# Performance work log

Measured on AMD Instinct MI355X. Metric: run time of the kernel, lower is better.

Reference implementation:

```python
import jax, jax.numpy as jnp
import numpy as np

N_DEPTH = 4
N_STACKS = 2
INPUT_SIZE = 1024
HIDDEN_SIZE = 4096
HU = HIDDEN_SIZE // (N_DEPTH * N_STACKS)  # unit_hidden_size = 512
BATCH = 4096


def setup_inputs() -> dict:
    key = jax.random.key(0)
    ks = jax.random.split(key, 8)
    inp = {
        "input": jax.random.normal(ks[0], (BATCH, INPUT_SIZE), dtype=jnp.float32),
        "state": jax.random.normal(ks[1], (2, N_STACKS, BATCH, HIDDEN_SIZE), dtype=jnp.float32),
        # LSTMCell params; residualStack=True -> every cell input dim = INPUT_SIZE
        "W_ih": jax.random.normal(ks[2], (N_DEPTH, N_STACKS, 4 * HU, INPUT_SIZE), dtype=jnp.float32) * 0.05,
        "W_hh": jax.random.normal(ks[3], (N_DEPTH, N_STACKS, 4 * HU, HU), dtype=jnp.float32) * 0.05,
        "b_ih": jax.random.normal(ks[4], (N_DEPTH, N_STACKS, 4 * HU), dtype=jnp.float32) * 0.05,
        "b_hh": jax.random.normal(ks[5], (N_DEPTH, N_STACKS, 4 * HU), dtype=jnp.float32) * 0.05,
        # stacks_proj: Linear(HU, INPUT_SIZE)
        "proj_W": jax.random.normal(ks[6], (INPUT_SIZE, HU), dtype=jnp.float32) * 0.05,
        "proj_b": jax.random.normal(ks[7], (INPUT_SIZE,), dtype=jnp.float32) * 0.05,
    }
    return inp


def _lstm_cell(x, hx, cx, w_ih, w_hh, b_ih, b_hh):
    # gates: [B, 4*HU], PyTorch LSTMCell gate order: i, f, g, o
    gates = x @ w_ih.T + b_ih + hx @ w_hh.T + b_hh
    i_g, f_g, g_g, o_g = jnp.split(gates, 4, axis=-1)
    i_g = jax.nn.sigmoid(i_g)
    f_g = jax.nn.sigmoid(f_g)
    g_g = jnp.tanh(g_g)
    o_g = jax.nn.sigmoid(o_g)
    c_out = f_g * cx + i_g * g_g
    h_out = o_g * jnp.tanh(c_out)
    return h_out, c_out


def reference(input, state, W_ih, W_hh, b_ih, b_hh, proj_W, proj_b):
    # residual=True, residualStack=True
    h_depth, c_depth = [], []
    for i in range(N_DEPTH):
        s, e = i * HU, (i + 1) * HU
        hs, cs = [], []
        dec_input = input
        h_out = None
        for j in range(N_STACKS):
            if j > 0:
                # residualStack: dec_input = dec_input + stacks_proj(h_out)
                dec_input = dec_input + h_out @ proj_W.T + proj_b
            hx = state[0, j, :, s:e]
            cx = state[1, j, :, s:e]
            h_out, c_out = _lstm_cell(dec_input, hx, cx,
                                      W_ih[i, j], W_hh[i, j], b_ih[i, j], b_hh[i, j])
            hs.append(h_out + hx)  # residual=True
            cs.append(c_out)
        h_depth.append(jnp.stack(hs, 0))  # [nStacks, B, HU]
        c_depth.append(jnp.stack(cs, 0))
    # hidden dim is laid out by depth slice: newState[..., i*HU:(i+1)*HU]
    newH = jnp.concatenate(h_depth, axis=-1)  # [nStacks, B, hidden_size]
    newC = jnp.concatenate(c_depth, axis=-1)
    newState = jnp.stack([newH, newC], axis=0)  # [2, nStacks, B, hidden_size]
    ho = newState[0, -1]  # [B, hidden_size]
    return ho, newState
```

## Files before the change

kernel.cpp:

```cpp
#include <hip/hip_runtime.h>
#include <cstdint>
#include <cstddef>

#define B_   4096
#define ISZ  1024
#define SW   4096
#define OHW  2048
#define HU_  512
#define NG   2048

typedef float f32x4 __attribute__((ext_vector_type(4)));
typedef short bf16x8 __attribute__((ext_vector_type(8)));

__device__ __forceinline__ short f2bf(float x) {
    union { float f; unsigned u; } v; v.f = x;
    unsigned r = v.u + 0x7fffu + ((v.u >> 16) & 1u);
    return (short)(r >> 16);
}
__device__ __forceinline__ float sigm(float x)   { return 1.f / (1.f + __expf(-x)); }
__device__ __forceinline__ float tanh_f(float x) { return 2.f / (1.f + __expf(-2.f * x)) - 1.f; }

__device__ __forceinline__ void async16(const void* g, void* l) {
    __builtin_amdgcn_global_load_lds((__attribute__((address_space(1))) void*)g,
                                     (__attribute__((address_space(3))) void*)l,
                                     16, 0, 0);
}

#define VM_BAR(N) asm volatile("s_waitcnt vmcnt(" #N ")\n\ts_barrier" ::: "memory")
#define BAR()     __builtin_amdgcn_s_barrier()

__global__ __launch_bounds__(256) void cvt_kernel(const float* __restrict__ src,
                                                  short* __restrict__ dst, long n) {
    long i = ((long)blockIdx.x * 256 + threadIdx.x) * 8;
    if (i >= n) return;
    float4 a = *(const float4*)(src + i);
    float4 b = *(const float4*)(src + i + 4);
    bf16x8 o;
    o[0] = f2bf(a.x); o[1] = f2bf(a.y); o[2] = f2bf(a.z); o[3] = f2bf(a.w);
    o[4] = f2bf(b.x); o[5] = f2bf(b.y); o[6] = f2bf(b.z); o[7] = f2bf(b.w);
    *(bf16x8*)(dst + i) = o;
}

__global__ __launch_bounds__(256) void cvt_h_kernel(const float* __restrict__ src,
                                                    short* __restrict__ dst) {
    long i = ((long)blockIdx.x * 256 + threadIdx.x) * 8;
    long row = i >> 11;
    long c   = i & 2047;
    const float* s = src + row * SW + c;
    float4 a = *(const float4*)(s);
    float4 b = *(const float4*)(s + 4);
    bf16x8 o;
    o[0] = f2bf(a.x); o[1] = f2bf(a.y); o[2] = f2bf(a.z); o[3] = f2bf(a.w);
    o[4] = f2bf(b.x); o[5] = f2bf(b.y); o[6] = f2bf(b.z); o[7] = f2bf(b.w);
    *(bf16x8*)(dst + i) = o;
}

#define MMA_BLK(BB, AR0, N0)                                                      \
  do {                                                                            \
    __builtin_amdgcn_s_setprio(1);                                                \
    _Pragma("unroll")                                                             \
    for (int mtl = 0; mtl < 4; ++mtl) {                                           \
      _Pragma("unroll")                                                           \
      for (int nn = 0; nn < 2; ++nn) {                                            \
        _Pragma("unroll")                                                         \
        for (int ks = 0; ks < 2; ++ks) {                                          \
          acc[(AR0) + mtl][(N0) + nn] = __builtin_amdgcn_mfma_f32_16x16x32_bf16(  \
              aR[mtl][ks], BB[nn][ks], acc[(AR0) + mtl][(N0) + nn], 0, 0, 0);     \
        }                                                                         \
      }                                                                           \
    }                                                                             \
    __builtin_amdgcn_s_setprio(0);                                                \
  } while (0)

#define GROW(rb) (((((rb) >> 4) & 3) << 9) + h0 + ((((rb) >> 6)) << 4) + ((rb) & 15))

__global__ __launch_bounds__(512, 2) void gates2_kernel(
    const short* __restrict__ A1, long a1_dstride,
    const short* __restrict__ Hb,
    const short* __restrict__ Wihb, const short* __restrict__ Whhb,
    const float* __restrict__ b_ih, const float* __restrict__ b_hh,
    const float* __restrict__ state,
    float* __restrict__ out_ho, float* __restrict__ out_state,
    short* __restrict__ h0b,
    int j)
{
    extern __shared__ short lds[];

    const int tid  = threadIdx.x;
    const int wave = tid >> 6;
    const int lane = tid & 63;
    const int wm   = wave >> 2;
    const int wn   = wave & 3;
    const int ln16 = lane & 15;
    const int q    = (lane >> 4) & 3;

    const int id  = blockIdx.x;
    const int swz = (id & 7) * 64 + (id >> 3);
    const int M0  = (swz & 15) * 256;
    const int h0  = ((swz >> 4) & 7) * 64;
    const int d   = swz >> 7;
    const int s   = d * HU_;

    const short* A1d = A1 + (size_t)d * a1_dstride;
    const short* A2  = Hb + (size_t)j * B_ * OHW + s;
    const short* W1  = Wihb + (size_t)(d * 2 + j) * NG * ISZ;
    const short* W2  = Whhb + (size_t)(d * 2 + j) * NG * HU_;
    const float* bi_ = b_ih + (size_t)(d * 2 + j) * NG;
    const float* bh_ = b_hh + (size_t)(d * 2 + j) * NG;

    const int srow = tid >> 3;
    const int scol = (((tid & 7) ^ ((tid >> 3) & 7)) << 3);

    const short* As = A1d;
    const short* Bs = W1;
    unsigned aoff0 = (unsigned)((M0 +   0 + srow) * ISZ + scol);
    unsigned aoff1 = (unsigned)((M0 +  64 + srow) * ISZ + scol);
    unsigned aoff2 = (unsigned)((M0 + 128 + srow) * ISZ + scol);
    unsigned aoff3 = (unsigned)((M0 + 192 + srow) * ISZ + scol);
    unsigned boff0 = (unsigned)(GROW(      srow) * ISZ + scol);
    unsigned boff1 = (unsigned)(GROW( 64 + srow) * ISZ + scol);
    unsigned boff2 = (unsigned)(GROW(128 + srow) * ISZ + scol);
    unsigned boff3 = (unsigned)(GROW(192 + srow) * ISZ + scol);

    const int swz0 = ((q    ) ^ (ln16 & 7)) << 4;
    const int swz1 = ((q + 4) ^ (ln16 & 7)) << 4;
    const char* ldsb = (const char*)lds;

    f32x4 acc[8][4];
#pragma unroll
    for (int i = 0; i < 8; ++i)
#pragma unroll
        for (int n = 0; n < 4; ++n) acc[i][n] = (f32x4){0.f, 0.f, 0.f, 0.f};

    bf16x8 aR[4][2];
    bf16x8 b01[2][2];
    bf16x8 b23[2][2];

    auto stA = [&](unsigned off, int it, int nbuf, int kofs) {
        async16(As + off + kofs, lds + nbuf * 32768 + (it * 64 + wave * 8) * 64);
    };
    auto stB = [&](unsigned off, int it, int nbuf, int kofs) {
        async16(Bs + off + kofs, lds + nbuf * 32768 + 16384 + (it * 64 + wave * 8) * 64);
    };
    auto rdA = [&](int buf, int hi) {
#pragma unroll
        for (int mtl = 0; mtl < 4; ++mtl) {
            const int row = wm * 128 + hi * 64 + mtl * 16 + ln16;
            aR[mtl][0] = *(const bf16x8*)(ldsb + buf * 65536 + row * 128 + swz0);
            aR[mtl][1] = *(const bf16x8*)(ldsb + buf * 65536 + row * 128 + swz1);
        }
    };
    auto rdB = [&](bf16x8 (&bb)[2][2], int buf, int nt0) {
#pragma unroll
        for (int nn = 0; nn < 2; ++nn) {
            const int row = wn * 64 + (nt0 + nn) * 16 + ln16;
            bb[nn][0] = *(const bf16x8*)(ldsb + buf * 65536 + 32768 + row * 128 + swz0);
            bb[nn][1] = *(const bf16x8*)(ldsb + buf * 65536 + 32768 + row * 128 + swz1);
        }
    };

    stB(boff0, 0, 0, 0); stB(boff1, 1, 0, 0); stB(boff2, 2, 0, 0); stB(boff3, 3, 0, 0);
    stA(aoff0, 0, 0, 0); stA(aoff2, 2, 0, 0);
    stA(aoff1, 1, 0, 0); stA(aoff3, 3, 0, 0);
    VM_BAR(2);

    auto do_tile = [&](int t, int kofs) {
        const int buf = t & 1, nbuf = buf ^ 1;
        rdA(buf, 0); rdB(b01, buf, 0);
        stB(boff0, 0, nbuf, kofs); stB(boff1, 1, nbuf, kofs);
        stB(boff2, 2, nbuf, kofs); stB(boff3, 3, nbuf, kofs);
        BAR();
        MMA_BLK(b01, 0, 0);
        BAR();
        rdB(b23, buf, 2);
        stA(aoff0, 0, nbuf, kofs); stA(aoff2, 2, nbuf, kofs);
        stA(aoff1, 1, nbuf, kofs); stA(aoff3, 3, nbuf, kofs);
        BAR();
        MMA_BLK(b23, 0, 2);
        VM_BAR(8);
        rdA(buf, 1);
        BAR();
        MMA_BLK(b23, 4, 2);
        BAR();
        MMA_BLK(b01, 4, 0);
        VM_BAR(2);
    };

    for (int t = 0; t < 15; ++t) do_tile(t, (t + 1) * 64);

    As = A2; Bs = W2;
    aoff0 = (unsigned)((M0 +   0 + srow) * OHW + scol);
    aoff1 = (unsigned)((M0 +  64 + srow) * OHW + scol);
    aoff2 = (unsigned)((M0 + 128 + srow) * OHW + scol);
    aoff3 = (unsigned)((M0 + 192 + srow) * OHW + scol);
    boff0 = (unsigned)(GROW(      srow) * HU_ + scol);
    boff1 = (unsigned)(GROW( 64 + srow) * HU_ + scol);
    boff2 = (unsigned)(GROW(128 + srow) * HU_ + scol);
    boff3 = (unsigned)(GROW(192 + srow) * HU_ + scol);

    for (int t = 15; t < 23; ++t) do_tile(t, (t - 15) * 64);

    {
        rdA(1, 0); rdB(b01, 1, 0);
        MMA_BLK(b01, 0, 0);
        rdB(b23, 1, 2);
        MMA_BLK(b23, 0, 2);
        VM_BAR(0);
        rdA(1, 1);
        MMA_BLK(b23, 4, 2);
        MMA_BLK(b01, 4, 0);
    }

    const int h   = h0 + wn * 16 + ln16;
    const int col = s + h;
    const float b_i = bi_[h]          + bh_[h];
    const float b_f = bi_[512 + h]    + bh_[512 + h];
    const float b_g = bi_[1024 + h]   + bh_[1024 + h];
    const float b_o = bi_[1536 + h]   + bh_[1536 + h];
#pragma unroll
    for (int mt = 0; mt < 8; ++mt) {
#pragma unroll
        for (int r = 0; r < 4; ++r) {
            const int m = M0 + wm * 128 + mt * 16 + q * 4 + r;
            const float hx = state[((size_t)(j)     * B_ + m) * SW + col];
            const float cx = state[((size_t)(2 + j) * B_ + m) * SW + col];
            const float gi = sigm(acc[mt][0][r] + b_i);
            const float gf = sigm(acc[mt][1][r] + b_f);
            const float gg = tanh_f(acc[mt][2][r] + b_g);
            const float go = sigm(acc[mt][3][r] + b_o);
            const float c_out = gf * cx + gi * gg;
            const float h_out = go * tanh_f(c_out);
            out_state[((size_t)(j)     * B_ + m) * OHW + col] = h_out + hx;
            out_state[((size_t)(2 + j) * B_ + m) * OHW + col] = c_out;
            if (j == 1) out_ho[(size_t)m * OHW + col] = h_out + hx;
            else        h0b[((size_t)d * B_ + m) * HU_ + h] = f2bf(h_out);
        }
    }
}

__global__ __launch_bounds__(256) void proj_kernel(
    const short* __restrict__ h0b, const short* __restrict__ PWb,
    const float* __restrict__ input, const float* __restrict__ proj_b,
    short* __restrict__ dec1b)
{
    __shared__ __align__(16) short sA[128 * 64];
    __shared__ __align__(16) short sB[128 * 64];

    const int t    = threadIdx.x;
    const int wave = t >> 6, lane = t & 63;
    const int ln16 = lane & 15, q = lane >> 4;
    const int d  = blockIdx.z;
    const int M0 = blockIdx.x * 128;
    const int N0 = blockIdx.y * 128;

    const short* A = h0b + (size_t)d * B_ * HU_;

    const int srow = wave * 8 + (lane >> 3);
    const int scol = (((lane & 7) ^ (lane >> 3)) << 3);

    f32x4 acc[2][8];
#pragma unroll
    for (int mt = 0; mt < 2; mt++)
#pragma unroll
        for (int nt = 0; nt < 8; nt++) acc[mt][nt] = (f32x4){0.f, 0.f, 0.f, 0.f};

    for (int k0 = 0; k0 < HU_; k0 += 64) {
#pragma unroll
        for (int it = 0; it < 4; it++)
            async16(A + (size_t)(M0 + it * 32 + srow) * HU_ + k0 + scol,
                    &sA[(it * 32 + wave * 8) * 64]);
#pragma unroll
        for (int it = 0; it < 4; it++)
            async16(PWb + (size_t)(N0 + it * 32 + srow) * HU_ + k0 + scol,
                    &sB[(it * 32 + wave * 8) * 64]);
        __syncthreads();
#pragma unroll
        for (int ks = 0; ks < 2; ks++) {
            const int kb = ks * 4 + q;
            bf16x8 a[2], b[8];
#pragma unroll
            for (int mt = 0; mt < 2; mt++) {
                const int m = wave * 32 + mt * 16 + ln16;
                a[mt] = *(const bf16x8*)&sA[m * 64 + ((kb ^ (m & 7)) << 3)];
            }
#pragma unroll
            for (int nt = 0; nt < 8; nt++) {
                const int n = nt * 16 + ln16;
                b[nt] = *(const bf16x8*)&sB[n * 64 + ((kb ^ (n & 7)) << 3)];
            }
#pragma unroll
            for (int mt = 0; mt < 2; mt++)
#pragma unroll
                for (int nt = 0; nt < 8; nt++)
                    acc[mt][nt] = __builtin_amdgcn_mfma_f32_16x16x32_bf16(a[mt], b[nt], acc[mt][nt], 0, 0, 0);
        }
        __syncthreads();
    }

#pragma unroll
    for (int mt = 0; mt < 2; mt++) {
#pragma unroll
        for (int nt = 0; nt < 8; nt++) {
            const int n = N0 + nt * 16 + ln16;
            const float pb = proj_b[n];
#pragma unroll
            for (int r = 0; r < 4; r++) {
                const int m = M0 + wave * 32 + mt * 16 + q * 4 + r;
                const float y = acc[mt][nt][r] + input[(size_t)m * ISZ + n] + pb;
                dec1b[((size_t)d * B_ + m) * ISZ + n] = f2bf(y);
            }
        }
    }
}

extern "C" void kernel_launch(void* const* d_in, const int* in_sizes, int n_in,
                              void* d_out, int out_size, void* d_ws, size_t ws_size,
                              hipStream_t stream)
{
    const float* input  = (const float*)d_in[0];
    const float* state  = (const float*)d_in[1];
    const float* W_ih   = (const float*)d_in[2];
    const float* W_hh   = (const float*)d_in[3];
    const float* b_ih   = (const float*)d_in[4];
    const float* b_hh   = (const float*)d_in[5];
    const float* proj_W = (const float*)d_in[6];
    const float* proj_b = (const float*)d_in[7];

    float* out_ho    = (float*)d_out;
    float* out_state = out_ho + (size_t)B_ * OHW;

    short* ws    = (short*)d_ws;
    short* Wihb  = ws;
    short* Whhb  = Wihb + (size_t)8 * NG * ISZ;
    short* PWb   = Whhb + (size_t)8 * NG * HU_;
    short* Hb    = PWb  + (size_t)ISZ * HU_;
    short* h0b   = Hb   + (size_t)2 * B_ * OHW;
    short* dec1b = h0b  + (size_t)4 * B_ * HU_;
    short* Xb    = dec1b;

    static bool s_attr = false;
    if (!s_attr) {
        (void)hipFuncSetAttribute(reinterpret_cast<const void*>(gates2_kernel),
                                  hipFuncAttributeMaxDynamicSharedMemorySize, 131072);
        s_attr = true;
    }

    {
        long n;
        n = (long)8 * NG * ISZ;  cvt_kernel<<<dim3((unsigned)(n / 8 / 256)), 256, 0, stream>>>(W_ih,   Wihb, n);
        n = (long)8 * NG * HU_;  cvt_kernel<<<dim3((unsigned)(n / 8 / 256)), 256, 0, stream>>>(W_hh,   Whhb, n);
        n = (long)ISZ * HU_;     cvt_kernel<<<dim3((unsigned)(n / 8 / 256)), 256, 0, stream>>>(proj_W, PWb,  n);
        n = (long)B_ * ISZ;      cvt_kernel<<<dim3((unsigned)(n / 8 / 256)), 256, 0, stream>>>(input,  Xb,   n);
        n = (long)2 * B_ * OHW;  cvt_h_kernel<<<dim3((unsigned)(n / 8 / 256)), 256, 0, stream>>>(state, Hb);
    }

    gates2_kernel<<<dim3(512), dim3(512), 131072, stream>>>(Xb, 0L, Hb, Wihb, Whhb,
                                                            b_ih, b_hh, state,
                                                            out_ho, out_state, h0b, 0);
    proj_kernel<<<dim3(32, 8, 4), 256, 0, stream>>>(h0b, PWb, input, proj_b, dec1b);
    gates2_kernel<<<dim3(512), dim3(512), 131072, stream>>>(dec1b, (long)B_ * ISZ, Hb, Wihb, Whhb,
                                                            b_ih, b_hh, state,
                                                            out_ho, out_state, nullptr, 1);
}
```

Before: 740.3 us.

## Rewrite projection GEMM with 256x256 tiles and double-buffered async LDS pipeline

Replaces the 128x128 single-buffered projection kernel with a 512-thread 256x256-tile kernel that double-buffers A and B tiles in 128KB of dynamic LDS. Global-to-LDS async loads for the next K slice are interleaved with MFMA blocks on the current slice, reusing the macros from the gates kernel. This is meant to hide load latency and raise operand reuse per LDS byte, at the cost of fewer blocks (256) and higher register and LDS pressure.

```diff
diff --git a/kernel.cpp b/kernel.cpp
--- a/kernel.cpp
+++ b/kernel.cpp
@@ -238,74 +238,127 @@
     }
 }
 
-__global__ __launch_bounds__(256) void proj_kernel(
+__global__ __launch_bounds__(512, 2) void proj2_kernel(
     const short* __restrict__ h0b, const short* __restrict__ PWb,
     const float* __restrict__ input, const float* __restrict__ proj_b,
     short* __restrict__ dec1b)
 {
-    __shared__ __align__(16) short sA[128 * 64];
-    __shared__ __align__(16) short sB[128 * 64];
-
-    const int t    = threadIdx.x;
-    const int wave = t >> 6, lane = t & 63;
-    const int ln16 = lane & 15, q = lane >> 4;
+    extern __shared__ short lds[];
+
+    const int tid  = threadIdx.x;
+    const int wave = tid >> 6;
+    const int lane = tid & 63;
+    const int wm   = wave >> 2;
+    const int wn   = wave & 3;
+    const int ln16 = lane & 15;
+    const int q    = (lane >> 4) & 3;
+
+    const int M0 = blockIdx.x * 256;
+    const int N0 = blockIdx.y * 256;
     const int d  = blockIdx.z;
-    const int M0 = blockIdx.x * 128;
-    const int N0 = blockIdx.y * 128;
-
-    const short* A = h0b + (size_t)d * B_ * HU_;
-
-    const int srow = wave * 8 + (lane >> 3);
-    const int scol = (((lane & 7) ^ (lane >> 3)) << 3);
-
-    f32x4 acc[2][8];
-#pragma unroll
-    for (int mt = 0; mt < 2; mt++)
-#pragma unroll
-        for (int nt = 0; nt < 8; nt++) acc[mt][nt] = (f32x4){0.f, 0.f, 0.f, 0.f};
-
-    for (int k0 = 0; k0 < HU_; k0 += 64) {
-#pragma unroll
-        for (int it = 0; it < 4; it++)
-            async16(A + (size_t)(M0 + it * 32 + srow) * HU_ + k0 + scol,
-                    &sA[(it * 32 + wave * 8) * 64]);
-#pragma unroll
-        for (int it = 0; it < 4; it++)
-            async16(PWb + (size_t)(N0 + it * 32 + srow) * HU_ + k0 + scol,
-                    &sB[(it * 32 + wave * 8) * 64]);
-        __syncthreads();
-#pragma unroll
-        for (int ks = 0; ks < 2; ks++) {
-            const int kb = ks * 4 + q;
-            bf16x8 a[2], b[8];
-#pragma unroll
-            for (int mt = 0; mt < 2; mt++) {
-                const int m = wave * 32 + mt * 16 + ln16;
-                a[mt] = *(const bf16x8*)&sA[m * 64 + ((kb ^ (m & 7)) << 3)];
-            }
-#pragma unroll
-            for (int nt = 0; nt < 8; nt++) {
-                const int n = nt * 16 + ln16;
-                b[nt] = *(const bf16x8*)&sB[n * 64 + ((kb ^ (n & 7)) << 3)];
-            }
-#pragma unroll
-            for (int mt = 0; mt < 2; mt++)
-#pragma unroll
-                for (int nt = 0; nt < 8; nt++)
-                    acc[mt][nt] = __builtin_amdgcn_mfma_f32_16x16x32_bf16(a[mt], b[nt], acc[mt][nt], 0, 0, 0);
-        }
-        __syncthreads();
-    }
-
-#pragma unroll
-    for (int mt = 0; mt < 2; mt++) {
-#pragma unroll
-        for (int nt = 0; nt < 8; nt++) {
-            const int n = N0 + nt * 16 + ln16;
+
+    const short* As = h0b + (size_t)d * B_ * HU_;
+    const short* Bs = PWb;
+
+    const int srow = tid >> 3;
+    const int scol = (((tid & 7) ^ ((tid >> 3) & 7)) << 3);
+
+    const unsigned aoff0 = (unsigned)((M0 +   0 + srow) * HU_ + scol);
+    const unsigned aoff1 = (unsigned)((M0 +  64 + srow) * HU_ + scol);
+    const unsigned aoff2 = (unsigned)((M0 + 128 + srow) * HU_ + scol);
+    const unsigned aoff3 = (unsigned)((M0 + 192 + srow) * HU_ + scol);
+    const unsigned boff0 = (unsigned)((N0 +   0 + srow) * HU_ + scol);
+    const unsigned boff1 = (unsigned)((N0 +  64 + srow) * HU_ + scol);
+    const unsigned boff2 = (unsigned)((N0 + 128 + srow) * HU_ + scol);
+    const unsigned boff3 = (unsigned)((N0 + 192 + srow) * HU_ + scol);
+
+    const int swz0 = ((q    ) ^ (ln16 & 7)) << 4;
+    const int swz1 = ((q + 4) ^ (ln16 & 7)) << 4;
+    const char* ldsb = (const char*)lds;
+
+    f32x4 acc[8][4];
+#pragma unroll
+    for (int i = 0; i < 8; ++i)
+#pragma unroll
+        for (int n = 0; n < 4; ++n) acc[i][n] = (f32x4){0.f, 0.f, 0.f, 0.f};
+
+    bf16x8 aR[4][2];
+    bf16x8 b01[2][2];
+    bf16x8 b23[2][2];
+
+    auto stA = [&](unsigned off, int it, int nbuf, int kofs) {
+        async16(As + off + kofs, lds + nbuf * 32768 + (it * 64 + wave * 8) * 64);
+    };
+    auto stB = [&](unsigned off, int it, int nbuf, int kofs) {
+        async16(Bs + off + kofs, lds + nbuf * 32768 + 16384 + (it * 64 + wave * 8) * 64);
+    };
+    auto rdA = [&](int buf, int hi) {
+#pragma unroll
+        for (int mtl = 0; mtl < 4; ++mtl) {
+            const int row = wm * 128 + hi * 64 + mtl * 16 + ln16;
+            aR[mtl][0] = *(const bf16x8*)(ldsb + buf * 65536 + row * 128 + swz0);
+            aR[mtl][1] = *(const bf16x8*)(ldsb + buf * 65536 + row * 128 + swz1);
+        }
+    };
+    auto rdB = [&](bf16x8 (&bb)[2][2], int buf, int nt0) {
+#pragma unroll
+        for (int nn = 0; nn < 2; ++nn) {
+            const int row = wn * 64 + (nt0 + nn) * 16 + ln16;
+            bb[nn][0] = *(const bf16x8*)(ldsb + buf * 65536 + 32768 + row * 128 + swz0);
+            bb[nn][1] = *(const bf16x8*)(ldsb + buf * 65536 + 32768 + row * 128 + swz1);
+        }
+    };
+
+    stB(boff0, 0, 0, 0); stB(boff1, 1, 0, 0); stB(boff2, 2, 0, 0); stB(boff3, 3, 0, 0);
+    stA(aoff0, 0, 0, 0); stA(aoff2, 2, 0, 0);
+    stA(aoff1, 1, 0, 0); stA(aoff3, 3, 0, 0);
+    VM_BAR(2);
+
+    auto do_tile = [&](int t, int kofs) {
+        const int buf = t & 1, nbuf = buf ^ 1;
+        rdA(buf, 0); rdB(b01, buf, 0);
+        stB(boff0, 0, nbuf, kofs); stB(boff1, 1, nbuf, kofs);
+        stB(boff2, 2, nbuf, kofs); stB(boff3, 3, nbuf, kofs);
+        BAR();
+        MMA_BLK(b01, 0, 0);
+        BAR();
+        rdB(b23, buf, 2);
+        stA(aoff0, 0, nbuf, kofs); stA(aoff2, 2, nbuf, kofs);
+        stA(aoff1, 1, nbuf, kofs); stA(aoff3, 3, nbuf, kofs);
+        BAR();
+        MMA_BLK(b23, 0, 2);
+        VM_BAR(8);
+        rdA(buf, 1);
+        BAR();
+        MMA_BLK(b23, 4, 2);
+        BAR();
+        MMA_BLK(b01, 4, 0);
+        VM_BAR(2);
+    };
+
+    for (int t = 0; t < 7; ++t) do_tile(t, (t + 1) * 64);
+
+    {
+        rdA(1, 0); rdB(b01, 1, 0);
+        MMA_BLK(b01, 0, 0);
+        rdB(b23, 1, 2);
+        MMA_BLK(b23, 0, 2);
+        VM_BAR(0);
+        rdA(1, 1);
+        MMA_BLK(b23, 4, 2);
+        MMA_BLK(b01, 4, 0);
+    }
+
+    const int nBase = N0 + wn * 64;
+#pragma unroll
+    for (int mt = 0; mt < 8; ++mt) {
+#pragma unroll
+        for (int nt = 0; nt < 4; ++nt) {
+            const int n = nBase + nt * 16 + ln16;
             const float pb = proj_b[n];
 #pragma unroll
-            for (int r = 0; r < 4; r++) {
-                const int m = M0 + wave * 32 + mt * 16 + q * 4 + r;
+            for (int r = 0; r < 4; ++r) {
+                const int m = M0 + wm * 128 + mt * 16 + q * 4 + r;
                 const float y = acc[mt][nt][r] + input[(size_t)m * ISZ + n] + pb;
                 dec1b[((size_t)d * B_ + m) * ISZ + n] = f2bf(y);
             }
@@ -342,6 +395,8 @@
     if (!s_attr) {
         (void)hipFuncSetAttribute(reinterpret_cast<const void*>(gates2_kernel),
                                   hipFuncAttributeMaxDynamicSharedMemorySize, 131072);
+        (void)hipFuncSetAttribute(reinterpret_cast<const void*>(proj2_kernel),
+                                  hipFuncAttributeMaxDynamicSharedMemorySize, 131072);
         s_attr = true;
     }
 
@@ -357,7 +412,7 @@
     gates2_kernel<<<dim3(512), dim3(512), 131072, stream>>>(Xb, 0L, Hb, Wihb, Whhb,
                                                             b_ih, b_hh, state,
                                                             out_ho, out_state, h0b, 0);
-    proj_kernel<<<dim3(32, 8, 4), 256, 0, stream>>>(h0b, PWb, input, proj_b, dec1b);
+    proj2_kernel<<<dim3(16, 4, 4), dim3(512), 131072, stream>>>(h0b, PWb, input, proj_b, dec1b);
     gates2_kernel<<<dim3(512), dim3(512), 131072, stream>>>(dec1b, (long)B_ * ISZ, Hb, Wihb, Whhb,
                                                             b_ih, b_hh, state,
                                                             out_ho, out_state, nullptr, 1);
```

After: 747.3 us. No clear change (+0.9%).
